# Performance work log

Measured on AMD Instinct MI355X. Metric: run time of the kernel, lower is better.

## Reference

```python
import jax, jax.numpy as jnp
import numpy as np

ENTROPY_TEMPERATURE = 0.01
ENTROPY_LOSS_RATIO = 0.1
BETA = 0.25  # commitment loss weight


def setup_inputs() -> dict:
    key = jax.random.key(0)
    k1, k2 = jax.random.split(key)
    z = jax.random.normal(k1, (32, 32, 16, 16), dtype=jnp.float32)
    # VQ codebook [K, C]
    embedding = jax.random.normal(k2, (16384, 32), dtype=jnp.float32) * 0.05
    return {"z": z, "embedding": embedding}


def _entropy_loss(affinity):
    # faithful to compute_entropy_loss(loss_type='softmax', temperature=0.01)
    flat = affinity.reshape(-1, affinity.shape[-1]) / ENTROPY_TEMPERATURE  # [N, K]
    probs = jax.nn.softmax(flat, axis=-1)
    log_probs = jax.nn.log_softmax(flat + 1e-5, axis=-1)
    avg_probs = jnp.mean(probs, axis=0)  # [K]
    avg_entropy = -jnp.sum(avg_probs * jnp.log(avg_probs + 1e-5))
    sample_entropy = -jnp.mean(jnp.sum(probs * log_probs, axis=-1))
    return sample_entropy - avg_entropy


def reference(z, embedding):
    B, C, H, W = z.shape
    zf = jnp.transpose(z, (0, 2, 3, 1)).reshape(-1, C)  # [N, C]
    # squared L2 distances to every codebook entry: [N, K]
    d = (jnp.sum(zf * zf, axis=1, keepdims=True)
         + jnp.sum(embedding * embedding, axis=1)
         - 2.0 * (zf @ embedding.T))
    idx = jnp.argmin(d, axis=1)                # [N] nearest codes
    z_q = jnp.take(embedding, idx, axis=0)     # [N, C]

    commit_loss = jnp.mean((jax.lax.stop_gradient(z_q) - zf) ** 2)
    codebook_loss = jnp.mean((z_q - jax.lax.stop_gradient(zf)) ** 2)
    ent_loss = _entropy_loss(-d)
    loss = codebook_loss + BETA * commit_loss + ENTROPY_LOSS_RATIO * ent_loss

    # straight-through estimator
    z_q_st = zf + jax.lax.stop_gradient(z_q - zf)
    z_q_out = jnp.transpose(z_q_st.reshape(B, H, W, C), (0, 3, 1, 2))  # [B, C, H, W]
    return z_q_out, loss, idx
```

## Files before the change

kernel.cpp:

```cpp
#include <hip/hip_runtime.h>

#define KCODES 16384
#define CDIM   32
#define NROWS  8192
#define KSPLIT 4
#define CHUNK  (KCODES/KSPLIT)
#define WCODES 1024
#define NT     (WCODES/16)
#define MARGIN 2.5f

typedef _Float16 half8 __attribute__((ext_vector_type(8)));
typedef float    floatx4 __attribute__((ext_vector_type(4)));

#define WS_MSE   0
#define WS_PLP   1
#define WS_AVGP  16
#define WS_ENORM (16 + KCODES)
#define WS_ZNORM (16 + 2*KCODES)
#define WS_PART  (16 + 2*KCODES + NROWS)
#define WS_E16   (WS_PART + 4*KSPLIT*NROWS)
#define WS_Z16   (WS_E16 + KCODES*16)

#define OUT_LOSS (NROWS*CDIM)
#define OUT_IDX  (NROWS*CDIM + 1)

__global__ __launch_bounds__(256) void prep_kernel(const float* __restrict__ z,
                                                   const float* __restrict__ emb,
                                                   float* __restrict__ ws) {
  const int tid = threadIdx.x;
  if (blockIdx.x < 64) {
    int k = blockIdx.x * 256 + tid;
    const float4* p = (const float4*)(emb + (size_t)k * CDIM);
    _Float16* e16 = (_Float16*)(ws + WS_E16);
    float s = 0.f;
    half8 h[4];
#pragma unroll
    for (int i = 0; i < 8; ++i) {
      float4 v = p[i];
      s += v.x*v.x + v.y*v.y + v.z*v.z + v.w*v.w;
      h[i>>1][(i&1)*4+0] = (_Float16)v.x;
      h[i>>1][(i&1)*4+1] = (_Float16)v.y;
      h[i>>1][(i&1)*4+2] = (_Float16)v.z;
      h[i>>1][(i&1)*4+3] = (_Float16)v.w;
    }
    ws[WS_ENORM + k] = s;
    ws[WS_AVGP + k]  = 0.f;
    half8* dst = (half8*)(e16 + (size_t)k*32);
#pragma unroll
    for (int i = 0; i < 4; ++i) dst[i] = h[i];
  } else {
    int b = blockIdx.x - 64;
    int n = b*256 + tid;
    if (b == 0 && tid < 16) ws[tid] = 0.f;
    _Float16* z16 = (_Float16*)(ws + WS_Z16);
    float s = 0.f;
    half8 h[4];
#pragma unroll
    for (int c = 0; c < CDIM; ++c) {
      float v = z[(size_t)b*8192 + c*256 + tid];
      s = fmaf(v, v, s);
      h[c>>3][c&7] = (_Float16)v;
    }
    ws[WS_ZNORM + n] = s;
    half8* dst = (half8*)(z16 + (size_t)n*32);
#pragma unroll
    for (int i = 0; i < 4; ++i) dst[i] = h[i];
  }
}

__global__ __launch_bounds__(256) void gemm_pass(const float* __restrict__ ws_ro,
                                                 float* __restrict__ ws) {
  __shared__ float2 dmp1[64][33];
  __shared__ float2 dmp2[64][33];
  __shared__ float4 d2[32][4];

  const int tid  = threadIdx.x;
  const int wv   = tid >> 6;
  const int lane = tid & 63;
  const int nn   = lane & 15;
  const int quad = lane >> 4;
  const int n0   = blockIdx.x * 32;
  const int kb   = blockIdx.y * CHUNK + wv * WCODES;

  const half8* z16v = (const half8*)(ws_ro + WS_Z16);
  const half8* e16v = (const half8*)(ws_ro + WS_E16);
  const float* enorm = ws_ro + WS_ENORM;
  const float* znorm = ws_ro + WS_ZNORM;
  float4* part = (float4*)(ws + WS_PART);

  half8 a0 = z16v[(size_t)(n0 + nn)*4 + quad];
  half8 a1 = z16v[(size_t)(n0 + 16 + nn)*4 + quad];

  float nzn2[8];
#pragma unroll
  for (int i = 0; i < 8; ++i)
    nzn2[i] = -0.5f * znorm[n0 + (i>>2)*16 + quad*4 + (i&3)];

  float t1l[8], t2l[8];
#pragma unroll
  for (int i = 0; i < 8; ++i) { t1l[i] = -3.0e38f; t2l[i] = -3.0e38f; }

  half8 bcur = e16v[(size_t)(kb + nn)*4 + quad];
  float en2c = 0.5f * enorm[kb + nn];

  for (int t = 0; t < NT; ++t) {
    const int tn = (t + 1 < NT) ? t + 1 : t;
    half8 bn   = e16v[(size_t)(kb + tn*16 + nn)*4 + quad];
    float en2n = 0.5f * enorm[kb + tn*16 + nn];

    floatx4 c0, c1;
#pragma unroll
    for (int i = 0; i < 4; ++i) { c0[i] = nzn2[i] - en2c; c1[i] = nzn2[i+4] - en2c; }

    floatx4 d0 = __builtin_amdgcn_mfma_f32_16x16x32_f16(a0, bcur, c0, 0, 0, 0);
    floatx4 d1 = __builtin_amdgcn_mfma_f32_16x16x32_f16(a1, bcur, c1, 0, 0, 0);

    const int tag = 63 - t;
#pragma unroll
    for (int i = 0; i < 8; ++i) {
      float lp = (i < 4) ? d0[i & 3] : d1[i & 3];
      float v  = __int_as_float((__float_as_int(lp) & 0xFFFFFFC0) | tag);
      t2l[i] = __builtin_amdgcn_fmed3f(v, t1l[i], t2l[i]);
      t1l[i] = fmaxf(t1l[i], v);
    }
    bcur = bn; en2c = en2n;
  }

  const int slot = wv*16 + nn;
#pragma unroll
  for (int i = 0; i < 8; ++i) {
    int row = (i>>2)*16 + quad*4 + (i&3);
    int c1i = kb + nn + 16*(63 - (__float_as_int(t1l[i]) & 63));
    int c2i = kb + nn + 16*(63 - (__float_as_int(t2l[i]) & 63));
    dmp1[slot][row] = make_float2(200.f*t1l[i], __int_as_float(c1i));
    dmp2[slot][row] = make_float2(200.f*t2l[i], __int_as_float(c2i));
  }
  __syncthreads();

  if (tid < 128) {
    int row = tid >> 2, seg = tid & 3;
    float bl0 = -3.0e38f, bl1 = -3.0e38f; int bc0 = 0, bc1 = 0;
#pragma unroll
    for (int s = 0; s < 16; ++s) {
      int sl = seg*16 + s;
#pragma unroll
      for (int q = 0; q < 2; ++q) {
        float2 pr = q ? dmp2[sl][row] : dmp1[sl][row];
        float pl = pr.x; int pc = __float_as_int(pr.y);
        if (pl > bl0 || (pl == bl0 && pc < bc0)) {
          bl1 = bl0; bc1 = bc0; bl0 = pl; bc0 = pc;
        } else if (pl > bl1 || (pl == bl1 && pc < bc1)) {
          bl1 = pl; bc1 = pc;
        }
      }
    }
    d2[row][seg] = make_float4(bl0, __int_as_float(bc0), bl1, __int_as_float(bc1));
  }
  __syncthreads();

  if (tid < 32) {
    float bl0 = -3.0e38f, bl1 = -3.0e38f; int bc0 = 0, bc1 = 0;
#pragma unroll
    for (int seg = 0; seg < 4; ++seg) {
      float4 v = d2[tid][seg];
#pragma unroll
      for (int q = 0; q < 2; ++q) {
        float pl = q ? v.z : v.x;
        int   pc = __float_as_int(q ? v.w : v.y);
        if (pl > bl0 || (pl == bl0 && pc < bc0)) {
          bl1 = bl0; bc1 = bc0; bl0 = pl; bc0 = pc;
        } else if (pl > bl1 || (pl == bl1 && pc < bc1)) {
          bl1 = pl; bc1 = pc;
        }
      }
    }
    part[(size_t)blockIdx.y*NROWS + n0 + tid] =
        make_float4(bl0, __int_as_float(bc0), bl1, __int_as_float(bc1));
  }
}

__global__ __launch_bounds__(256) void combine_kernel(const float* __restrict__ z,
                                                      const float* __restrict__ emb,
                                                      float* __restrict__ ws,
                                                      float* __restrict__ out) {
  const float4* part = (const float4*)(ws + WS_PART);
  int n = blockIdx.x*256 + threadIdx.x;

  float l[8]; int c[8];
#pragma unroll
  for (int ch = 0; ch < KSPLIT; ++ch) {
    float4 v = part[(size_t)ch*NROWS + n];
    l[ch*2+0] = v.x; c[ch*2+0] = __float_as_int(v.y);
    l[ch*2+1] = v.z; c[ch*2+1] = __float_as_int(v.w);
  }
  float mm = l[0];
#pragma unroll
  for (int i = 1; i < 8; ++i) mm = fmaxf(mm, l[i]);

  int bb = n >> 8, hw = n & 255;
  float zr[32];
  float zn = 0.f;
#pragma unroll
  for (int cc = 0; cc < CDIM; ++cc) {
    zr[cc] = z[(size_t)bb*8192 + cc*256 + hw];
    zn = fmaf(zr[cc], zr[cc], zn);
  }
  float bd = 3.0e38f; int bc = 0x7fffffff;
#pragma unroll
  for (int i = 0; i < 8; ++i) {
    if (l[i] > mm - MARGIN) {
      int code = c[i];
      const float* er = emb + (size_t)code*CDIM;
      float dot = 0.f;
#pragma unroll
      for (int cc = 0; cc < CDIM; ++cc) dot = fmaf(zr[cc], er[cc], dot);
      float d = (zn + ws[WS_ENORM + code]) - 2.f*dot;
      if (d < bd || (d == bd && code < bc)) { bd = d; bc = code; }
    }
  }
  out[OUT_IDX + n] = (float)bc;

  const float* er = emb + (size_t)bc*CDIM;
  float msel = 0.f;
#pragma unroll
  for (int cc = 0; cc < CDIM; ++cc) {
    float zq = er[cc];
    float df = zq - zr[cc];
    msel = fmaf(df, df, msel);
    out[(size_t)bb*8192 + cc*256 + hw] = zr[cc] + (zq - zr[cc]);
  }
  for (int off = 1; off < 64; off <<= 1) msel += __shfl_xor(msel, off);
  if ((threadIdx.x & 63) == 0) atomicAdd(&ws[WS_MSE], msel);

  float s = 0.f;
#pragma unroll
  for (int i = 0; i < 8; ++i) s += __expf(l[i] - mm);
  float lse = mm + __logf(s);

  float plp = 0.f;
#pragma unroll
  for (int i = 0; i < 8; ++i) {
    float u = l[i] - lse;
    float p = __expf(u);
    plp = fmaf(p, u, plp);
    if (p > 1e-12f) atomicAdd(&ws[WS_AVGP + c[i]], p);
  }
  for (int off = 1; off < 64; off <<= 1) plp += __shfl_xor(plp, off);
  if ((threadIdx.x & 63) == 0) atomicAdd(&ws[WS_PLP], plp);
}

__global__ __launch_bounds__(256) void finalize_kernel(const float* __restrict__ ws,
                                                       float* __restrict__ out) {
  __shared__ float red[256];
  float h = 0.f;
  for (int k = threadIdx.x; k < KCODES; k += 256) {
    float ap = ws[WS_AVGP + k] * (1.f/8192.f);
    h += ap * __logf(ap + 1e-5f);
  }
  red[threadIdx.x] = h;
  __syncthreads();
  for (int st = 128; st > 0; st >>= 1) {
    if (threadIdx.x < st) red[threadIdx.x] += red[threadIdx.x + st];
    __syncthreads();
  }
  if (threadIdx.x == 0) {
    float mse        = ws[WS_MSE] * (1.f/(8192.f*32.f));
    float sample_ent = -ws[WS_PLP] * (1.f/8192.f);
    out[OUT_LOSS] = 1.25f*mse + 0.1f*(sample_ent + red[0]);
  }
}

extern "C" void kernel_launch(void* const* d_in, const int* in_sizes, int n_in,
                              void* d_out, int out_size, void* d_ws, size_t ws_size,
                              hipStream_t stream) {
  (void)in_sizes; (void)n_in; (void)out_size; (void)ws_size;
  const float* z   = (const float*)d_in[0];
  const float* emb = (const float*)d_in[1];
  float* out = (float*)d_out;
  float* ws  = (float*)d_ws;

  prep_kernel    <<<96, 256, 0, stream>>>(z, emb, ws);
  gemm_pass      <<<dim3(NROWS/32, KSPLIT), 256, 0, stream>>>(ws, ws);
  combine_kernel <<<NROWS/256, 256, 0, stream>>>(z, emb, ws, out);
  finalize_kernel<<<1, 256, 0, stream>>>(ws, out);
}
```

Baseline: 132.7 us.

## Split codebook 8-way, pack code index in low bits, shuffle-based top-2 reduction

Doubles the K split of the distance GEMM so twice as many blocks run, each with a shorter code loop. The full 12-bit in-chunk code index now goes into the low mantissa bits, so the top-2 can be merged with warp shuffles and one small LDS pass instead of two shared-memory reduction stages. The combine kernel switches to 64-thread blocks, takes 16 candidates per row, uses a wider rescoring margin, and loads embeddings as float4. Truncating 12 mantissa bits coarsens the approximate logits used for the entropy term and for candidate screening, and the WS_PART buffer is now read over 8 slices.

Measured after the change: 131.9 us. About the same (-0.6%).

```diff
diff --git a/kernel.cpp b/kernel.cpp
--- a/kernel.cpp
+++ b/kernel.cpp
@@ -3,11 +3,11 @@
 #define KCODES 16384
 #define CDIM   32
 #define NROWS  8192
-#define KSPLIT 4
+#define KSPLIT 8
 #define CHUNK  (KCODES/KSPLIT)
-#define WCODES 1024
+#define WCODES (CHUNK/4)
 #define NT     (WCODES/16)
-#define MARGIN 2.5f
+#define MARGIN 4.0f
 
 typedef _Float16 half8 __attribute__((ext_vector_type(8)));
 typedef float    floatx4 __attribute__((ext_vector_type(4)));
@@ -70,9 +70,7 @@
 
 __global__ __launch_bounds__(256) void gemm_pass(const float* __restrict__ ws_ro,
                                                  float* __restrict__ ws) {
-  __shared__ float2 dmp1[64][33];
-  __shared__ float2 dmp2[64][33];
-  __shared__ float4 d2[32][4];
+  __shared__ float2 wdump[4][32];
 
   const int tid  = threadIdx.x;
   const int wv   = tid >> 6;
@@ -100,6 +98,7 @@
 #pragma unroll
   for (int i = 0; i < 8; ++i) { t1l[i] = -3.0e38f; t2l[i] = -3.0e38f; }
 
+  const int tagbase = wv*WCODES + nn;
   half8 bcur = e16v[(size_t)(kb + nn)*4 + quad];
   float en2c = 0.5f * enorm[kb + nn];
 
@@ -115,78 +114,59 @@
     floatx4 d0 = __builtin_amdgcn_mfma_f32_16x16x32_f16(a0, bcur, c0, 0, 0, 0);
     floatx4 d1 = __builtin_amdgcn_mfma_f32_16x16x32_f16(a1, bcur, c1, 0, 0, 0);
 
-    const int tag = 63 - t;
+    const int tg = tagbase + 16*t;
 #pragma unroll
     for (int i = 0; i < 8; ++i) {
       float lp = (i < 4) ? d0[i & 3] : d1[i & 3];
-      float v  = __int_as_float((__float_as_int(lp) & 0xFFFFFFC0) | tag);
+      float v  = __int_as_float((__float_as_int(lp) & 0xFFFFF000) | tg);
       t2l[i] = __builtin_amdgcn_fmed3f(v, t1l[i], t2l[i]);
       t1l[i] = fmaxf(t1l[i], v);
     }
     bcur = bn; en2c = en2n;
   }
 
-  const int slot = wv*16 + nn;
 #pragma unroll
   for (int i = 0; i < 8; ++i) {
-    int row = (i>>2)*16 + quad*4 + (i&3);
-    int c1i = kb + nn + 16*(63 - (__float_as_int(t1l[i]) & 63));
-    int c2i = kb + nn + 16*(63 - (__float_as_int(t2l[i]) & 63));
-    dmp1[slot][row] = make_float2(200.f*t1l[i], __int_as_float(c1i));
-    dmp2[slot][row] = make_float2(200.f*t2l[i], __int_as_float(c2i));
+    float v1 = t1l[i], v2 = t2l[i];
+#pragma unroll
+    for (int m = 1; m < 16; m <<= 1) {
+      float o1 = __shfl_xor(v1, m);
+      float o2 = __shfl_xor(v2, m);
+      float mn = fminf(v1, o1);
+      v1 = fmaxf(v1, o1);
+      v2 = fmaxf(mn, fmaxf(v2, o2));
+    }
+    if (nn == 0) wdump[wv][(i>>2)*16 + quad*4 + (i&3)] = make_float2(v1, v2);
   }
   __syncthreads();
 
-  if (tid < 128) {
-    int row = tid >> 2, seg = tid & 3;
-    float bl0 = -3.0e38f, bl1 = -3.0e38f; int bc0 = 0, bc1 = 0;
-#pragma unroll
-    for (int s = 0; s < 16; ++s) {
-      int sl = seg*16 + s;
-#pragma unroll
-      for (int q = 0; q < 2; ++q) {
-        float2 pr = q ? dmp2[sl][row] : dmp1[sl][row];
-        float pl = pr.x; int pc = __float_as_int(pr.y);
-        if (pl > bl0 || (pl == bl0 && pc < bc0)) {
-          bl1 = bl0; bc1 = bc0; bl0 = pl; bc0 = pc;
-        } else if (pl > bl1 || (pl == bl1 && pc < bc1)) {
-          bl1 = pl; bc1 = pc;
-        }
-      }
-    }
-    d2[row][seg] = make_float4(bl0, __int_as_float(bc0), bl1, __int_as_float(bc1));
-  }
-  __syncthreads();
-
   if (tid < 32) {
-    float bl0 = -3.0e38f, bl1 = -3.0e38f; int bc0 = 0, bc1 = 0;
-#pragma unroll
-    for (int seg = 0; seg < 4; ++seg) {
-      float4 v = d2[tid][seg];
-#pragma unroll
-      for (int q = 0; q < 2; ++q) {
-        float pl = q ? v.z : v.x;
-        int   pc = __float_as_int(q ? v.w : v.y);
-        if (pl > bl0 || (pl == bl0 && pc < bc0)) {
-          bl1 = bl0; bc1 = bc0; bl0 = pl; bc0 = pc;
-        } else if (pl > bl1 || (pl == bl1 && pc < bc1)) {
-          bl1 = pl; bc1 = pc;
-        }
-      }
-    }
+    float v1 = -3.0e38f, v2 = -3.0e38f;
+#pragma unroll
+    for (int w = 0; w < 4; ++w) {
+      float2 p = wdump[w][tid];
+      float mn = fminf(v1, p.x);
+      v1 = fmaxf(v1, p.x);
+      v2 = fmaxf(mn, fmaxf(v2, p.y));
+    }
+    int b1 = __float_as_int(v1), b2 = __float_as_int(v2);
+    int c1i = blockIdx.y*CHUNK + (b1 & 0xFFF);
+    int c2i = blockIdx.y*CHUNK + (b2 & 0xFFF);
+    float l1 = 200.f * __int_as_float(b1 & 0xFFFFF000);
+    float l2 = 200.f * __int_as_float(b2 & 0xFFFFF000);
     part[(size_t)blockIdx.y*NROWS + n0 + tid] =
-        make_float4(bl0, __int_as_float(bc0), bl1, __int_as_float(bc1));
-  }
-}
-
-__global__ __launch_bounds__(256) void combine_kernel(const float* __restrict__ z,
-                                                      const float* __restrict__ emb,
-                                                      float* __restrict__ ws,
-                                                      float* __restrict__ out) {
+        make_float4(l1, __int_as_float(c1i), l2, __int_as_float(c2i));
+  }
+}
+
+__global__ __launch_bounds__(64) void combine_kernel(const float* __restrict__ z,
+                                                     const float* __restrict__ emb,
+                                                     float* __restrict__ ws,
+                                                     float* __restrict__ out) {
   const float4* part = (const float4*)(ws + WS_PART);
-  int n = blockIdx.x*256 + threadIdx.x;
-
-  float l[8]; int c[8];
+  int n = blockIdx.x*64 + threadIdx.x;
+
+  float l[16]; int c[16];
 #pragma unroll
   for (int ch = 0; ch < KSPLIT; ++ch) {
     float4 v = part[(size_t)ch*NROWS + n];
@@ -195,7 +175,7 @@
   }
   float mm = l[0];
 #pragma unroll
-  for (int i = 1; i < 8; ++i) mm = fmaxf(mm, l[i]);
+  for (int i = 1; i < 16; ++i) mm = fmaxf(mm, l[i]);
 
   int bb = n >> 8, hw = n & 255;
   float zr[32];
@@ -207,13 +187,19 @@
   }
   float bd = 3.0e38f; int bc = 0x7fffffff;
 #pragma unroll
-  for (int i = 0; i < 8; ++i) {
+  for (int i = 0; i < 16; ++i) {
     if (l[i] > mm - MARGIN) {
       int code = c[i];
-      const float* er = emb + (size_t)code*CDIM;
+      const float4* er4 = (const float4*)(emb + (size_t)code*CDIM);
       float dot = 0.f;
 #pragma unroll
-      for (int cc = 0; cc < CDIM; ++cc) dot = fmaf(zr[cc], er[cc], dot);
+      for (int q = 0; q < 8; ++q) {
+        float4 e4 = er4[q];
+        dot = fmaf(zr[q*4+0], e4.x, dot);
+        dot = fmaf(zr[q*4+1], e4.y, dot);
+        dot = fmaf(zr[q*4+2], e4.z, dot);
+        dot = fmaf(zr[q*4+3], e4.w, dot);
+      }
       float d = (zn + ws[WS_ENORM + code]) - 2.f*dot;
       if (d < bd || (d == bd && code < bc)) { bd = d; bc = code; }
     }
@@ -230,23 +216,23 @@
     out[(size_t)bb*8192 + cc*256 + hw] = zr[cc] + (zq - zr[cc]);
   }
   for (int off = 1; off < 64; off <<= 1) msel += __shfl_xor(msel, off);
-  if ((threadIdx.x & 63) == 0) atomicAdd(&ws[WS_MSE], msel);
+  if (threadIdx.x == 0) atomicAdd(&ws[WS_MSE], msel);
 
   float s = 0.f;
 #pragma unroll
-  for (int i = 0; i < 8; ++i) s += __expf(l[i] - mm);
+  for (int i = 0; i < 16; ++i) s += __expf(l[i] - mm);
   float lse = mm + __logf(s);
 
   float plp = 0.f;
 #pragma unroll
-  for (int i = 0; i < 8; ++i) {
+  for (int i = 0; i < 16; ++i) {
     float u = l[i] - lse;
     float p = __expf(u);
     plp = fmaf(p, u, plp);
     if (p > 1e-12f) atomicAdd(&ws[WS_AVGP + c[i]], p);
   }
   for (int off = 1; off < 64; off <<= 1) plp += __shfl_xor(plp, off);
-  if ((threadIdx.x & 63) == 0) atomicAdd(&ws[WS_PLP], plp);
+  if (threadIdx.x == 0) atomicAdd(&ws[WS_PLP], plp);
 }
 
 __global__ __launch_bounds__(256) void finalize_kernel(const float* __restrict__ ws,
@@ -281,6 +267,6 @@
 
   prep_kernel    <<<96, 256, 0, stream>>>(z, emb, ws);
   gemm_pass      <<<dim3(NROWS/32, KSPLIT), 256, 0, stream>>>(ws, ws);
-  combine_kernel <<<NROWS/256, 256, 0, stream>>>(z, emb, ws, out);
+  combine_kernel <<<NROWS/64, 64, 0, stream>>>(z, emb, ws, out);
   finalize_kernel<<<1, 256, 0, stream>>>(ws, out);
 }
```
